# Performance work log

Measured on AMD Instinct MI355X. Metric: run time of the kernel, lower is better.

The kernel has to match this reference:

```python
import jax, jax.numpy as jnp
import numpy as np

N_NODES = 10000
N_EDGES = 640000
NODE_DIM = 128
EDGE_DIM = 32
OUT_DIM = 128


def setup_inputs() -> dict:
    key = jax.random.key(0)
    k_h, k_e, k_ef, k_w1, k_w2 = jax.random.split(key, 5)
    h = jax.random.normal(k_h, (N_NODES, NODE_DIM), dtype=jnp.float32)
    edge_index = jax.random.randint(k_e, (2, N_EDGES), 0, N_NODES, dtype=jnp.int64)
    edge_features = jax.random.normal(k_ef, (N_EDGES, EDGE_DIM), dtype=jnp.float32)
    in_dim = 2 * NODE_DIM + EDGE_DIM
    # Kaiming-ish init scale for realism
    W1 = jax.random.normal(k_w1, (in_dim, OUT_DIM), dtype=jnp.float32) / np.sqrt(in_dim)
    b1 = jnp.zeros((OUT_DIM,), dtype=jnp.float32)
    W2 = jax.random.normal(k_w2, (OUT_DIM, OUT_DIM), dtype=jnp.float32) / np.sqrt(OUT_DIM)
    b2 = jnp.zeros((OUT_DIM,), dtype=jnp.float32)
    return {"h": h, "edge_index": edge_index, "edge_features": edge_features,
            "n": N_NODES, "W1": W1, "b1": b1, "W2": W2, "b2": b2}


def reference(h, edge_index, edge_features, n, W1, b1, W2, b2):
    rows, cols = edge_index[0], edge_index[1]
    # gather source/target node features + edge features -> [E, 2*node_dim+edge_dim]
    msg_input = jnp.concatenate([h[rows], h[cols], edge_features], axis=-1)
    hidden = jax.nn.relu(msg_input @ W1 + b1)   # [E, out_dim]
    messages = hidden @ W2 + b2                 # [E, out_dim]
    # scatter-add messages onto destination rows -> [n, out_dim]
    out = jax.ops.segment_sum(messages, rows, num_segments=n)
    return out
```

## Files before the change

kernel.cpp:

```cpp
#include <hip/hip_runtime.h>
#include <hip/hip_bf16.h>


typedef __attribute__((ext_vector_type(8))) short bf16x8;
typedef __attribute__((ext_vector_type(4))) float f32x4;

#define ND 128
#define ED 32
#define CH 64
#define INV_WSCALE 0.0625f

__device__ __forceinline__ short f2bf(float x) {
  unsigned int u = __float_as_uint(x);
  unsigned int r = (u + 0x7FFFu + ((u >> 16) & 1u)) >> 16;
  return (short)r;
}

__device__ __forceinline__ float bf2f(short s) {
  return __uint_as_float(((unsigned int)(unsigned short)s) << 16);
}

__device__ __forceinline__ f32x4 bf8lo(bf16x8 v) {
  f32x4 r;
  #pragma unroll
  for (int j = 0; j < 4; ++j) r[j] = bf2f(v[j]);
  return r;
}
__device__ __forceinline__ f32x4 bf8hi(bf16x8 v) {
  f32x4 r;
  #pragma unroll
  for (int j = 0; j < 4; ++j) r[j] = bf2f(v[4 + j]);
  return r;
}

__device__ __forceinline__ int pk_fp8x4(float a, float b, float c, float d) {
  int w = __builtin_amdgcn_cvt_pk_fp8_f32(a, b, 0, false);
  w = __builtin_amdgcn_cvt_pk_fp8_f32(c, d, w, true);
  return w;
}

__device__ __forceinline__ int swz(int c) {
  int ct = c >> 4, cc = c & 15;
  return (ct >> 2) * 64 + (cc >> 2) * 16 + (ct & 3) * 4 + (cc & 3);
}

__global__ __launch_bounds__(256) void prep_hist_kernel(
    const float* __restrict__ W1, const float* __restrict__ W2,
    const void* __restrict__ ei, int* __restrict__ counts,
    unsigned int* __restrict__ rc, short* __restrict__ w12t,
    long long* __restrict__ w1eA8, short* __restrict__ w2t, int E) {
  int b = blockIdx.x;
  if (b < 128) {
    int t = b * 256 + threadIdx.x;
    if (t < 256 * 128) {
      int np = t >> 7, k = t & 127;
      float v = (np < 128) ? W1[k * 128 + np] : W1[(128 + k) * 128 + (np - 128)];
      w12t[t] = f2bf(v);
    }
    if (t < 128 * 128) {
      int n = t >> 7, k = t & 127;
      w2t[t] = f2bf(W2[k * 128 + n]);
    }
    if (t < 8 * 64) {
      int ct = t >> 6, lane = t & 63;
      int li = lane & 15, lg = lane >> 4;
      float v[8];
      #pragma unroll
      for (int j = 0; j < 8; ++j)
        v[j] = W1[(256 + lg * 8 + j) * 128 + ct * 16 + li] * 16.f;
      int lo = pk_fp8x4(v[0], v[1], v[2], v[3]);
      int hi = pk_fp8x4(v[4], v[5], v[6], v[7]);
      w1eA8[ct * 64 + lane] = (long long)(unsigned int)lo |
                              ((long long)(unsigned int)hi << 32);
    }
  } else {
    int e = (b - 128) * 256 + threadIdx.x;
    if (e < E) {
      const unsigned int* u = (const unsigned int*)ei;
      int is64 = 1;
      #pragma unroll
      for (int i = 0; i < 16; ++i)
        if (u[2 * i + 1] != 0u) is64 = 0;
      int r, c;
      if (is64) {
        r = (int)((const long long*)ei)[e];
        c = (int)((const long long*)ei)[(long long)E + e];
      } else {
        r = ((const int*)ei)[e];
        c = ((const int*)ei)[E + e];
      }
      atomicAdd(&counts[r], 1);
      rc[e] = ((unsigned int)r << 16) | (unsigned int)c;
    }
  }
}

__global__ __launch_bounds__(1024) void scan_kernel(const int* __restrict__ counts,
                                                    int* __restrict__ row_ptr,
                                                    int* __restrict__ cur, int n) {
  __shared__ int wtot[16];
  int tid = threadIdx.x;
  int lane = tid & 63, w = tid >> 6;
  int base_i = tid * 16;
  int c[16];
  int tot = 0;
  #pragma unroll
  for (int j = 0; j < 16; ++j) {
    int i = base_i + j;
    c[j] = (i < n) ? counts[i] : 0;
    tot += c[j];
  }
  int x = tot;
  #pragma unroll
  for (int d = 1; d < 64; d <<= 1) {
    int t = __shfl_up(x, d);
    if (lane >= d) x += t;
  }
  if (lane == 63) wtot[w] = x;
  __syncthreads();
  if (w == 0) {
    int y = (lane < 16) ? wtot[lane] : 0;
    #pragma unroll
    for (int d = 1; d < 16; d <<= 1) {
      int t = __shfl_up(y, d);
      if (lane >= d) y += t;
    }
    if (lane < 16) wtot[lane] = y;
  }
  __syncthreads();
  int waveoff = (w == 0) ? 0 : wtot[w - 1];
  int run = waveoff + x - tot;
  if (tid == 0) row_ptr[0] = 0;
  #pragma unroll
  for (int j = 0; j < 16; ++j) {
    int i = base_i + j;
    if (i < n) {
      cur[i] = run;
      run += c[j];
      row_ptr[i + 1] = run;
    }
  }
}

__global__ __launch_bounds__(256, 4) void scatter_sg_kernel(
    const float* __restrict__ ef, const int* __restrict__ row_ptr,
    int* __restrict__ cur, const unsigned int* __restrict__ rc,
    const float* __restrict__ h, const short* __restrict__ w12t,
    const float* __restrict__ b1, unsigned char* __restrict__ efb,
    unsigned short* __restrict__ ccol, int2* __restrict__ cb,
    float* __restrict__ s2, short* __restrict__ g2, int N, int E, int nchunks) {
  int b = blockIdx.x;
  int SGB = (N + 63) >> 6;
  int SCB = (2 * E + 255) >> 8;
  if (b < SGB) {
    int lane = threadIdx.x & 63, w = threadIdx.x >> 6;
    int li = lane & 15, lg = lane >> 4;
    int base = b * 64 + w * 16;
    int rowm = base + li;
    if (rowm >= N) rowm = N - 1;
    float breg[8];
    #pragma unroll
    for (int nt = 0; nt < 8; ++nt) breg[nt] = b1[nt * 16 + li];
    f32x4 acc[16];
    #pragma unroll
    for (int nt = 0; nt < 16; ++nt) acc[nt] = (f32x4){0.f, 0.f, 0.f, 0.f};
    #pragma unroll
    for (int kc = 0; kc < 4; ++kc) {
      f32x4 f0 = *(const f32x4*)(h + (size_t)rowm * ND + kc * 32 + lg * 8);
      f32x4 f1 = *(const f32x4*)(h + (size_t)rowm * ND + kc * 32 + lg * 8 + 4);
      bf16x8 a;
      #pragma unroll
      for (int j = 0; j < 4; ++j) { a[j] = f2bf(f0[j]); a[4 + j] = f2bf(f1[j]); }
      #pragma unroll
      for (int nt = 0; nt < 16; ++nt) {
        bf16x8 bb = *(const bf16x8*)(w12t + (nt * 16 + li) * 128 + kc * 32 + lg * 8);
        acc[nt] = __builtin_amdgcn_mfma_f32_16x16x32_bf16(a, bb, acc[nt], 0, 0, 0);
      }
    }
    #pragma unroll
    for (int nt = 0; nt < 16; ++nt)
      #pragma unroll
      for (int r = 0; r < 4; ++r) {
        int row = base + lg * 4 + r;
        if (row < N) {
          if (nt < 8) {
            s2[(size_t)row * 128 + swz(nt * 16 + li)] = acc[nt][r] + breg[nt];
          } else {
            g2[(size_t)row * 128 + swz((nt - 8) * 16 + li)] = f2bf(acc[nt][r]);
          }
        }
      }
  } else if (b < SGB + SCB) {
    int gt = (b - SGB) * 256 + threadIdx.x;
    int e = gt >> 1, part = gt & 1;
    if (e < E) {
      unsigned int p = rc[e];
      int r = (int)(p >> 16), c = (int)(p & 0xffffu);
      int pos0 = 0;
      if (part == 0) pos0 = atomicAdd(&cur[r], 1);
      int lane = threadIdx.x & 63;
      int pos = __shfl(pos0, lane - part);
      const float* ep = ef + (size_t)e * ED + part * 16;
      f32x4 x0 = *(const f32x4*)(ep);
      f32x4 x1 = *(const f32x4*)(ep + 4);
      f32x4 x2 = *(const f32x4*)(ep + 8);
      f32x4 x3 = *(const f32x4*)(ep + 12);
      int4 ob;
      ob.x = pk_fp8x4(x0[0], x0[1], x0[2], x0[3]);
      ob.y = pk_fp8x4(x1[0], x1[1], x1[2], x1[3]);
      ob.z = pk_fp8x4(x2[0], x2[1], x2[2], x2[3]);
      ob.w = pk_fp8x4(x3[0], x3[1], x3[2], x3[3]);
      *(int4*)(efb + (size_t)pos * ED + part * 16) = ob;
      if (part == 0) ccol[pos] = (unsigned short)c;
    }
  } else {
    int k = (b - SGB - SCB) * 256 + threadIdx.x;
    if (k < nchunks) {
      int t0 = k * CH, t1 = t0 + CH;
      int lo = 0, hi = N;
      while (lo < hi) { int mid = (lo + hi) >> 1; if (row_ptr[mid] < t0) lo = mid + 1; else hi = mid; }
      int na = lo;
      hi = N;
      while (lo < hi) { int mid = (lo + hi) >> 1; if (row_ptr[mid] < t1) lo = mid + 1; else hi = mid; }
      cb[k] = make_int2(na, lo);
    }
  }
}

__global__ __launch_bounds__(128, 4) void layer1_kernel(
    const float* __restrict__ s2, const short* __restrict__ g2,
    const unsigned char* __restrict__ efb, const unsigned short* __restrict__ ccol,
    const long long* __restrict__ w1eA8, const int* __restrict__ row_ptr,
    const int2* __restrict__ cb, float* __restrict__ hsum) {
  int2 bounds = cb[blockIdx.x];
  int na = bounds.x, nb = bounds.y;
  if (na >= nb) return;
  int lane = threadIdx.x & 63;
  int w = threadIdx.x >> 6;
  int li = lane & 15, lg = lane >> 4;

  long long wa[4];
  #pragma unroll
  for (int nt = 0; nt < 4; ++nt)
    wa[nt] = w1eA8[(w * 4 + nt) * 64 + lane];

  for (int n = na; n < nb; ++n) {
    int rp = row_ptr[n], rpe = row_ptr[n + 1];
    int deg = rpe - rp;
    f32x4 sreg[4];
    #pragma unroll
    for (int nt = 0; nt < 4; ++nt)
      sreg[nt] = *(const f32x4*)(s2 + (size_t)n * 128 + w * 64 + lg * 16 + nt * 4);
    f32x4 psum[4];
    #pragma unroll
    for (int nt = 0; nt < 4; ++nt) psum[nt] = (f32x4){0.f, 0.f, 0.f, 0.f};

    int ntiles = (deg + 15) >> 4;
    int last = rpe - 1;
    auto ldpos = [&](int t) {
      int p = rp + t * 16 + li;
      return p > last ? last : p;
    };

    int pA = ldpos(0), pB = ldpos(1);
    int cA = ccol[pA], cB = ccol[pB];
    long long eA = *(const long long*)(efb + (size_t)pA * ED + lg * 8);
    long long eB = *(const long long*)(efb + (size_t)pB * ED + lg * 8);
    const short* gpA = g2 + (size_t)cA * 128 + w * 64 + lg * 16;
    bf16x8 gA0 = *(const bf16x8*)gpA;
    bf16x8 gA1 = *(const bf16x8*)(gpA + 8);

    for (int t = 0; t < ntiles; ++t) {
      const short* gpB = g2 + (size_t)cB * 128 + w * 64 + lg * 16;
      bf16x8 gB0 = *(const bf16x8*)gpB;
      bf16x8 gB1 = *(const bf16x8*)(gpB + 8);
      int pC = ldpos(t + 2);
      int cC = ccol[pC];
      long long eC = *(const long long*)(efb + (size_t)pC * ED + lg * 8);
      f32x4 a0 = __builtin_amdgcn_mfma_f32_16x16x32_fp8_fp8(wa[0], eA, (f32x4){0.f,0.f,0.f,0.f}, 0, 0, 0);
      f32x4 a1 = __builtin_amdgcn_mfma_f32_16x16x32_fp8_fp8(wa[1], eA, (f32x4){0.f,0.f,0.f,0.f}, 0, 0, 0);
      f32x4 a2 = __builtin_amdgcn_mfma_f32_16x16x32_fp8_fp8(wa[2], eA, (f32x4){0.f,0.f,0.f,0.f}, 0, 0, 0);
      f32x4 a3 = __builtin_amdgcn_mfma_f32_16x16x32_fp8_fp8(wa[3], eA, (f32x4){0.f,0.f,0.f,0.f}, 0, 0, 0);
      if ((t * 16 + li) < deg) {
        f32x4 g0 = bf8lo(gA0), g1 = bf8hi(gA0), g2v = bf8lo(gA1), g3 = bf8hi(gA1);
        #pragma unroll
        for (int r = 0; r < 4; ++r) {
          float v0 = fmaf(a0[r], INV_WSCALE, sreg[0][r] + g0[r]);
          float v1 = fmaf(a1[r], INV_WSCALE, sreg[1][r] + g1[r]);
          float v2 = fmaf(a2[r], INV_WSCALE, sreg[2][r] + g2v[r]);
          float v3 = fmaf(a3[r], INV_WSCALE, sreg[3][r] + g3[r]);
          psum[0][r] += (v0 > 0.f ? v0 : 0.f);
          psum[1][r] += (v1 > 0.f ? v1 : 0.f);
          psum[2][r] += (v2 > 0.f ? v2 : 0.f);
          psum[3][r] += (v3 > 0.f ? v3 : 0.f);
        }
      }
      cB = cC; eA = eB; eB = eC;
      gA0 = gB0; gA1 = gB1;
    }

    #pragma unroll
    for (int nt = 0; nt < 4; ++nt)
      #pragma unroll
      for (int r = 0; r < 4; ++r) {
        float v = psum[nt][r];
        v += __shfl_xor(v, 1);
        v += __shfl_xor(v, 2);
        v += __shfl_xor(v, 4);
        v += __shfl_xor(v, 8);
        psum[nt][r] = v;
      }
    if (li == 0) {
      #pragma unroll
      for (int nt = 0; nt < 4; ++nt)
        *(f32x4*)(hsum + (size_t)n * 128 + w * 64 + nt * 16 + lg * 4) = psum[nt];
    }
  }
}

__global__ __launch_bounds__(256) void out_kernel(const float* __restrict__ hsum,
                                                  const short* __restrict__ w2t,
                                                  const float* __restrict__ b2,
                                                  const int* __restrict__ row_ptr,
                                                  float* __restrict__ out, int N) {
  int lane = threadIdx.x & 63, w = threadIdx.x >> 6;
  int li = lane & 15, lg = lane >> 4;
  int base = blockIdx.x * 64 + w * 16;
  int rowm = base + li;
  if (rowm >= N) rowm = N - 1;
  float breg[8];
  #pragma unroll
  for (int nt = 0; nt < 8; ++nt) breg[nt] = b2[nt * 16 + li];
  f32x4 acc[8];
  #pragma unroll
  for (int nt = 0; nt < 8; ++nt) acc[nt] = (f32x4){0.f, 0.f, 0.f, 0.f};
  #pragma unroll
  for (int kc = 0; kc < 4; ++kc) {
    f32x4 f0 = *(const f32x4*)(hsum + (size_t)rowm * 128 + kc * 32 + lg * 8);
    f32x4 f1 = *(const f32x4*)(hsum + (size_t)rowm * 128 + kc * 32 + lg * 8 + 4);
    bf16x8 a;
    #pragma unroll
    for (int j = 0; j < 4; ++j) { a[j] = f2bf(f0[j]); a[4 + j] = f2bf(f1[j]); }
    #pragma unroll
    for (int nt = 0; nt < 8; ++nt) {
      bf16x8 bb = *(const bf16x8*)(w2t + (nt * 16 + li) * 128 + kc * 32 + lg * 8);
      acc[nt] = __builtin_amdgcn_mfma_f32_16x16x32_bf16(a, bb, acc[nt], 0, 0, 0);
    }
  }
  #pragma unroll
  for (int r = 0; r < 4; ++r) {
    int row = base + lg * 4 + r;
    if (row < N) {
      float dg = (float)(row_ptr[row + 1] - row_ptr[row]);
      #pragma unroll
      for (int nt = 0; nt < 8; ++nt)
        out[(size_t)row * 128 + nt * 16 + li] = acc[nt][r] + dg * breg[nt];
    }
  }
}

extern "C" void kernel_launch(void* const* d_in, const int* in_sizes, int n_in,
                              void* d_out, int out_size, void* d_ws, size_t ws_size,
                              hipStream_t stream) {
  const float* h  = (const float*)d_in[0];
  const void*  ei = d_in[1];
  const float* ef = (const float*)d_in[2];
  const float* W1 = (const float*)d_in[4];
  const float* b1 = (const float*)d_in[5];
  const float* W2 = (const float*)d_in[6];
  const float* b2 = (const float*)d_in[7];
  float* out = (float*)d_out;
  int N = in_sizes[0] / ND;
  int E = in_sizes[2] / ED;
  int nchunks = (E + CH - 1) / CH;

  char* ws = (char*)d_ws;
  size_t off = 0;
  auto alloc = [&](size_t bytes) {
    size_t o = off;
    off = (off + bytes + 255) & ~(size_t)255;
    return o;
  };
  int*            counts  = (int*)(ws + alloc((size_t)N * 4));
  int*            row_ptr = (int*)(ws + alloc((size_t)(N + 1) * 4));
  int*            cur     = (int*)(ws + alloc((size_t)N * 4));
  unsigned int*   rc      = (unsigned int*)(ws + alloc((size_t)E * 4));
  short*          w12t    = (short*)(ws + alloc(256 * 128 * 2));
  long long*      w1eA8   = (long long*)(ws + alloc(8 * 64 * 8));
  short*          w2t     = (short*)(ws + alloc(128 * 128 * 2));
  float*          s2      = (float*)(ws + alloc((size_t)N * 128 * 4));
  short*          g2      = (short*)(ws + alloc((size_t)N * 128 * 2));
  float*          hsumb   = (float*)(ws + alloc((size_t)N * 128 * 4));
  unsigned char*  efb     = (unsigned char*)(ws + alloc((size_t)E * ED));
  unsigned short* ccol    = (unsigned short*)(ws + alloc((size_t)E * 2));
  int2*           cbb     = (int2*)(ws + alloc((size_t)nchunks * 8));

  int SGB = (N + 63) >> 6;
  int SCB = (2 * E + 255) >> 8;
  int CBB = (nchunks + 255) >> 8;

  hipMemsetAsync(counts, 0, (size_t)N * 4, stream);
  prep_hist_kernel<<<128 + (E + 255) / 256, 256, 0, stream>>>(
      W1, W2, ei, counts, rc, w12t, w1eA8, w2t, E);
  scan_kernel<<<1, 1024, 0, stream>>>(counts, row_ptr, cur, N);
  scatter_sg_kernel<<<SGB + SCB + CBB, 256, 0, stream>>>(
      ef, row_ptr, cur, rc, h, w12t, b1, efb, ccol, cbb, s2, g2, N, E, nchunks);
  layer1_kernel<<<nchunks, 128, 0, stream>>>(s2, g2, efb, ccol, w1eA8, row_ptr, cbb, hsumb);
  out_kernel<<<(N + 63) / 64, 256, 0, stream>>>(hsumb, w2t, b2, row_ptr, out, N);
}
```

Measured before the change: 158.7 us.

## Use histogram ranks for CSR placement, pack edge records, one block per node

The histogram atomic now also returns each edge's rank within its row. The scatter pass computes its CSR position as row_ptr[r]+rank[e], which removes the second atomicAdd pass over a cursor array. Edge features (fp8) and the column index are packed into one 64-byte record so layer1 reads them together. Layer1 now launches one block per node instead of edge-count chunks, which drops the binary-search chunk-bounds step. In exchange it writes an extra rank array and doubles edge-record size, with 28 bytes of zero padding per record, which adds memory traffic.

```diff
diff --git a/kernel.cpp b/kernel.cpp
--- a/kernel.cpp
+++ b/kernel.cpp
@@ -7,7 +7,7 @@
 
 #define ND 128
 #define ED 32
-#define CH 64
+#define RECB 64
 #define INV_WSCALE 0.0625f
 
 __device__ __forceinline__ short f2bf(float x) {
@@ -47,8 +47,9 @@
 __global__ __launch_bounds__(256) void prep_hist_kernel(
     const float* __restrict__ W1, const float* __restrict__ W2,
     const void* __restrict__ ei, int* __restrict__ counts,
-    unsigned int* __restrict__ rc, short* __restrict__ w12t,
-    long long* __restrict__ w1eA8, short* __restrict__ w2t, int E) {
+    int* __restrict__ rank, unsigned int* __restrict__ rc,
+    short* __restrict__ w12t, long long* __restrict__ w1eA8,
+    short* __restrict__ w2t, int E) {
   int b = blockIdx.x;
   if (b < 128) {
     int t = b * 256 + threadIdx.x;
@@ -89,15 +90,14 @@
         r = ((const int*)ei)[e];
         c = ((const int*)ei)[E + e];
       }
-      atomicAdd(&counts[r], 1);
+      rank[e] = atomicAdd(&counts[r], 1);
       rc[e] = ((unsigned int)r << 16) | (unsigned int)c;
     }
   }
 }
 
 __global__ __launch_bounds__(1024) void scan_kernel(const int* __restrict__ counts,
-                                                    int* __restrict__ row_ptr,
-                                                    int* __restrict__ cur, int n) {
+                                                    int* __restrict__ row_ptr, int n) {
   __shared__ int wtot[16];
   int tid = threadIdx.x;
   int lane = tid & 63, w = tid >> 6;
@@ -135,7 +135,6 @@
   for (int j = 0; j < 16; ++j) {
     int i = base_i + j;
     if (i < n) {
-      cur[i] = run;
       run += c[j];
       row_ptr[i + 1] = run;
     }
@@ -144,14 +143,12 @@
 
 __global__ __launch_bounds__(256, 4) void scatter_sg_kernel(
     const float* __restrict__ ef, const int* __restrict__ row_ptr,
-    int* __restrict__ cur, const unsigned int* __restrict__ rc,
+    const int* __restrict__ rank, const unsigned int* __restrict__ rc,
     const float* __restrict__ h, const short* __restrict__ w12t,
     const float* __restrict__ b1, unsigned char* __restrict__ efb,
-    unsigned short* __restrict__ ccol, int2* __restrict__ cb,
-    float* __restrict__ s2, short* __restrict__ g2, int N, int E, int nchunks) {
+    float* __restrict__ s2, short* __restrict__ g2, int N, int E) {
   int b = blockIdx.x;
   int SGB = (N + 63) >> 6;
-  int SCB = (2 * E + 255) >> 8;
   if (b < SGB) {
     int lane = threadIdx.x & 63, w = threadIdx.x >> 6;
     int li = lane & 15, lg = lane >> 4;
@@ -190,16 +187,13 @@
           }
         }
       }
-  } else if (b < SGB + SCB) {
+  } else {
     int gt = (b - SGB) * 256 + threadIdx.x;
     int e = gt >> 1, part = gt & 1;
     if (e < E) {
       unsigned int p = rc[e];
       int r = (int)(p >> 16), c = (int)(p & 0xffffu);
-      int pos0 = 0;
-      if (part == 0) pos0 = atomicAdd(&cur[r], 1);
-      int lane = threadIdx.x & 63;
-      int pos = __shfl(pos0, lane - part);
+      int pos = row_ptr[r] + rank[e];
       const float* ep = ef + (size_t)e * ED + part * 16;
       f32x4 x0 = *(const f32x4*)(ep);
       f32x4 x1 = *(const f32x4*)(ep + 4);
@@ -210,111 +204,109 @@
       ob.y = pk_fp8x4(x1[0], x1[1], x1[2], x1[3]);
       ob.z = pk_fp8x4(x2[0], x2[1], x2[2], x2[3]);
       ob.w = pk_fp8x4(x3[0], x3[1], x3[2], x3[3]);
-      *(int4*)(efb + (size_t)pos * ED + part * 16) = ob;
-      if (part == 0) ccol[pos] = (unsigned short)c;
-    }
-  } else {
-    int k = (b - SGB - SCB) * 256 + threadIdx.x;
-    if (k < nchunks) {
-      int t0 = k * CH, t1 = t0 + CH;
-      int lo = 0, hi = N;
-      while (lo < hi) { int mid = (lo + hi) >> 1; if (row_ptr[mid] < t0) lo = mid + 1; else hi = mid; }
-      int na = lo;
-      hi = N;
-      while (lo < hi) { int mid = (lo + hi) >> 1; if (row_ptr[mid] < t1) lo = mid + 1; else hi = mid; }
-      cb[k] = make_int2(na, lo);
+      unsigned char* rec = efb + (size_t)pos * RECB;
+      *(int4*)(rec + part * 16) = ob;
+      *(int4*)(rec + 32 + part * 16) = make_int4(part == 0 ? c : 0, 0, 0, 0);
     }
   }
 }
 
 __global__ __launch_bounds__(128, 4) void layer1_kernel(
     const float* __restrict__ s2, const short* __restrict__ g2,
-    const unsigned char* __restrict__ efb, const unsigned short* __restrict__ ccol,
-    const long long* __restrict__ w1eA8, const int* __restrict__ row_ptr,
-    const int2* __restrict__ cb, float* __restrict__ hsum) {
-  int2 bounds = cb[blockIdx.x];
-  int na = bounds.x, nb = bounds.y;
-  if (na >= nb) return;
+    const unsigned char* __restrict__ efb, const long long* __restrict__ w1eA8,
+    const int* __restrict__ row_ptr, float* __restrict__ hsum) {
+  int node = blockIdx.x;
   int lane = threadIdx.x & 63;
   int w = threadIdx.x >> 6;
   int li = lane & 15, lg = lane >> 4;
+  int rp = row_ptr[node], rpe = row_ptr[node + 1];
+  int deg = rpe - rp;
+
+  if (deg == 0) {
+    if (li == 0) {
+      #pragma unroll
+      for (int nt = 0; nt < 4; ++nt)
+        *(f32x4*)(hsum + (size_t)node * 128 + w * 64 + nt * 16 + lg * 4) =
+            (f32x4){0.f, 0.f, 0.f, 0.f};
+    }
+    return;
+  }
 
   long long wa[4];
   #pragma unroll
   for (int nt = 0; nt < 4; ++nt)
     wa[nt] = w1eA8[(w * 4 + nt) * 64 + lane];
-
-  for (int n = na; n < nb; ++n) {
-    int rp = row_ptr[n], rpe = row_ptr[n + 1];
-    int deg = rpe - rp;
-    f32x4 sreg[4];
+  f32x4 sreg[4];
+  #pragma unroll
+  for (int nt = 0; nt < 4; ++nt)
+    sreg[nt] = *(const f32x4*)(s2 + (size_t)node * 128 + w * 64 + lg * 16 + nt * 4);
+  f32x4 psum[4];
+  #pragma unroll
+  for (int nt = 0; nt < 4; ++nt) psum[nt] = (f32x4){0.f, 0.f, 0.f, 0.f};
+
+  int ntiles = (deg + 15) >> 4;
+  int last = rpe - 1;
+  auto ldpos = [&](int t) {
+    int p = rp + t * 16 + li;
+    return p > last ? last : p;
+  };
+
+  const unsigned char* recA = efb + (size_t)ldpos(0) * RECB;
+  const unsigned char* recB = efb + (size_t)ldpos(1) * RECB;
+  long long eA = *(const long long*)(recA + lg * 8);
+  int cA = *(const int*)(recA + 32);
+  long long eB = *(const long long*)(recB + lg * 8);
+  int cB = *(const int*)(recB + 32);
+  const short* gpA = g2 + (size_t)cA * 128 + w * 64 + lg * 16;
+  bf16x8 gA0 = *(const bf16x8*)gpA;
+  bf16x8 gA1 = *(const bf16x8*)(gpA + 8);
+
+  for (int t = 0; t < ntiles; ++t) {
+    const short* gpB = g2 + (size_t)cB * 128 + w * 64 + lg * 16;
+    bf16x8 gB0 = *(const bf16x8*)gpB;
+    bf16x8 gB1 = *(const bf16x8*)(gpB + 8);
+    const unsigned char* recC = efb + (size_t)ldpos(t + 2) * RECB;
+    long long eC = *(const long long*)(recC + lg * 8);
+    int cC = *(const int*)(recC + 32);
+    f32x4 a0 = __builtin_amdgcn_mfma_f32_16x16x32_fp8_fp8(wa[0], eA, (f32x4){0.f,0.f,0.f,0.f}, 0, 0, 0);
+    f32x4 a1 = __builtin_amdgcn_mfma_f32_16x16x32_fp8_fp8(wa[1], eA, (f32x4){0.f,0.f,0.f,0.f}, 0, 0, 0);
+    f32x4 a2 = __builtin_amdgcn_mfma_f32_16x16x32_fp8_fp8(wa[2], eA, (f32x4){0.f,0.f,0.f,0.f}, 0, 0, 0);
+    f32x4 a3 = __builtin_amdgcn_mfma_f32_16x16x32_fp8_fp8(wa[3], eA, (f32x4){0.f,0.f,0.f,0.f}, 0, 0, 0);
+    if ((t * 16 + li) < deg) {
+      f32x4 g0 = bf8lo(gA0), g1 = bf8hi(gA0), g2v = bf8lo(gA1), g3 = bf8hi(gA1);
+      #pragma unroll
+      for (int r = 0; r < 4; ++r) {
+        float v0 = fmaf(a0[r], INV_WSCALE, sreg[0][r] + g0[r]);
+        float v1 = fmaf(a1[r], INV_WSCALE, sreg[1][r] + g1[r]);
+        float v2 = fmaf(a2[r], INV_WSCALE, sreg[2][r] + g2v[r]);
+        float v3 = fmaf(a3[r], INV_WSCALE, sreg[3][r] + g3[r]);
+        psum[0][r] += (v0 > 0.f ? v0 : 0.f);
+        psum[1][r] += (v1 > 0.f ? v1 : 0.f);
+        psum[2][r] += (v2 > 0.f ? v2 : 0.f);
+        psum[3][r] += (v3 > 0.f ? v3 : 0.f);
+      }
+    }
+    eA = eB; cB2: ;
+    eB = eC;
+    cA = cB; cB = cC;
+    gA0 = gB0; gA1 = gB1;
+  }
+
+  #pragma unroll
+  for (int nt = 0; nt < 4; ++nt)
+    #pragma unroll
+    for (int r = 0; r < 4; ++r) {
+      float v = psum[nt][r];
+      v += __shfl_xor(v, 1);
+      v += __shfl_xor(v, 2);
+      v += __shfl_xor(v, 4);
+      v += __shfl_xor(v, 8);
+      psum[nt][r] = v;
+    }
+  if (li == 0) {
     #pragma unroll
     for (int nt = 0; nt < 4; ++nt)
-      sreg[nt] = *(const f32x4*)(s2 + (size_t)n * 128 + w * 64 + lg * 16 + nt * 4);
-    f32x4 psum[4];
-    #pragma unroll
-    for (int nt = 0; nt < 4; ++nt) psum[nt] = (f32x4){0.f, 0.f, 0.f, 0.f};
-
-    int ntiles = (deg + 15) >> 4;
-    int last = rpe - 1;
-    auto ldpos = [&](int t) {
-      int p = rp + t * 16 + li;
-      return p > last ? last : p;
-    };
-
-    int pA = ldpos(0), pB = ldpos(1);
-    int cA = ccol[pA], cB = ccol[pB];
-    long long eA = *(const long long*)(efb + (size_t)pA * ED + lg * 8);
-    long long eB = *(const long long*)(efb + (size_t)pB * ED + lg * 8);
-    const short* gpA = g2 + (size_t)cA * 128 + w * 64 + lg * 16;
-    bf16x8 gA0 = *(const bf16x8*)gpA;
-    bf16x8 gA1 = *(const bf16x8*)(gpA + 8);
-
-    for (int t = 0; t < ntiles; ++t) {
-      const short* gpB = g2 + (size_t)cB * 128 + w * 64 + lg * 16;
-      bf16x8 gB0 = *(const bf16x8*)gpB;
-      bf16x8 gB1 = *(const bf16x8*)(gpB + 8);
-      int pC = ldpos(t + 2);
-      int cC = ccol[pC];
-      long long eC = *(const long long*)(efb + (size_t)pC * ED + lg * 8);
-      f32x4 a0 = __builtin_amdgcn_mfma_f32_16x16x32_fp8_fp8(wa[0], eA, (f32x4){0.f,0.f,0.f,0.f}, 0, 0, 0);
-      f32x4 a1 = __builtin_amdgcn_mfma_f32_16x16x32_fp8_fp8(wa[1], eA, (f32x4){0.f,0.f,0.f,0.f}, 0, 0, 0);
-      f32x4 a2 = __builtin_amdgcn_mfma_f32_16x16x32_fp8_fp8(wa[2], eA, (f32x4){0.f,0.f,0.f,0.f}, 0, 0, 0);
-      f32x4 a3 = __builtin_amdgcn_mfma_f32_16x16x32_fp8_fp8(wa[3], eA, (f32x4){0.f,0.f,0.f,0.f}, 0, 0, 0);
-      if ((t * 16 + li) < deg) {
-        f32x4 g0 = bf8lo(gA0), g1 = bf8hi(gA0), g2v = bf8lo(gA1), g3 = bf8hi(gA1);
-        #pragma unroll
-        for (int r = 0; r < 4; ++r) {
-          float v0 = fmaf(a0[r], INV_WSCALE, sreg[0][r] + g0[r]);
-          float v1 = fmaf(a1[r], INV_WSCALE, sreg[1][r] + g1[r]);
-          float v2 = fmaf(a2[r], INV_WSCALE, sreg[2][r] + g2v[r]);
-          float v3 = fmaf(a3[r], INV_WSCALE, sreg[3][r] + g3[r]);
-          psum[0][r] += (v0 > 0.f ? v0 : 0.f);
-          psum[1][r] += (v1 > 0.f ? v1 : 0.f);
-          psum[2][r] += (v2 > 0.f ? v2 : 0.f);
-          psum[3][r] += (v3 > 0.f ? v3 : 0.f);
-        }
-      }
-      cB = cC; eA = eB; eB = eC;
-      gA0 = gB0; gA1 = gB1;
-    }
-
-    #pragma unroll
-    for (int nt = 0; nt < 4; ++nt)
-      #pragma unroll
-      for (int r = 0; r < 4; ++r) {
-        float v = psum[nt][r];
-        v += __shfl_xor(v, 1);
-        v += __shfl_xor(v, 2);
-        v += __shfl_xor(v, 4);
-        v += __shfl_xor(v, 8);
-        psum[nt][r] = v;
-      }
-    if (li == 0) {
-      #pragma unroll
-      for (int nt = 0; nt < 4; ++nt)
-        *(f32x4*)(hsum + (size_t)n * 128 + w * 64 + nt * 16 + lg * 4) = psum[nt];
-    }
+      *(f32x4*)(hsum + (size_t)node * 128 + w * 64 + nt * 16 + lg * 4) = psum[nt];
   }
 }
 
@@ -372,7 +364,6 @@
   float* out = (float*)d_out;
   int N = in_sizes[0] / ND;
   int E = in_sizes[2] / ED;
-  int nchunks = (E + CH - 1) / CH;
 
   char* ws = (char*)d_ws;
   size_t off = 0;
@@ -381,30 +372,27 @@
     off = (off + bytes + 255) & ~(size_t)255;
     return o;
   };
-  int*            counts  = (int*)(ws + alloc((size_t)N * 4));
-  int*            row_ptr = (int*)(ws + alloc((size_t)(N + 1) * 4));
-  int*            cur     = (int*)(ws + alloc((size_t)N * 4));
-  unsigned int*   rc      = (unsigned int*)(ws + alloc((size_t)E * 4));
-  short*          w12t    = (short*)(ws + alloc(256 * 128 * 2));
-  long long*      w1eA8   = (long long*)(ws + alloc(8 * 64 * 8));
-  short*          w2t     = (short*)(ws + alloc(128 * 128 * 2));
-  float*          s2      = (float*)(ws + alloc((size_t)N * 128 * 4));
-  short*          g2      = (short*)(ws + alloc((size_t)N * 128 * 2));
-  float*          hsumb   = (float*)(ws + alloc((size_t)N * 128 * 4));
-  unsigned char*  efb     = (unsigned char*)(ws + alloc((size_t)E * ED));
-  unsigned short* ccol    = (unsigned short*)(ws + alloc((size_t)E * 2));
-  int2*           cbb     = (int2*)(ws + alloc((size_t)nchunks * 8));
+  int*           counts  = (int*)(ws + alloc((size_t)N * 4));
+  int*           row_ptr = (int*)(ws + alloc((size_t)(N + 1) * 4));
+  int*           rank    = (int*)(ws + alloc((size_t)E * 4));
+  unsigned int*  rc      = (unsigned int*)(ws + alloc((size_t)E * 4));
+  short*         w12t    = (short*)(ws + alloc(256 * 128 * 2));
+  long long*     w1eA8   = (long long*)(ws + alloc(8 * 64 * 8));
+  short*         w2t     = (short*)(ws + alloc(128 * 128 * 2));
+  float*         s2      = (float*)(ws + alloc((size_t)N * 128 * 4));
+  short*         g2      = (short*)(ws + alloc((size_t)N * 128 * 2));
+  float*         hsumb   = (float*)(ws + alloc((size_t)N * 128 * 4));
+  unsigned char* efb     = (unsigned char*)(ws + alloc((size_t)E * RECB));
 
   int SGB = (N + 63) >> 6;
   int SCB = (2 * E + 255) >> 8;
-  int CBB = (nchunks + 255) >> 8;
 
   hipMemsetAsync(counts, 0, (size_t)N * 4, stream);
   prep_hist_kernel<<<128 + (E + 255) / 256, 256, 0, stream>>>(
-      W1, W2, ei, counts, rc, w12t, w1eA8, w2t, E);
-  scan_kernel<<<1, 1024, 0, stream>>>(counts, row_ptr, cur, N);
-  scatter_sg_kernel<<<SGB + SCB + CBB, 256, 0, stream>>>(
-      ef, row_ptr, cur, rc, h, w12t, b1, efb, ccol, cbb, s2, g2, N, E, nchunks);
-  layer1_kernel<<<nchunks, 128, 0, stream>>>(s2, g2, efb, ccol, w1eA8, row_ptr, cbb, hsumb);
+      W1, W2, ei, counts, rank, rc, w12t, w1eA8, w2t, E);
+  scan_kernel<<<1, 1024, 0, stream>>>(counts, row_ptr, N);
+  scatter_sg_kernel<<<SGB + SCB, 256, 0, stream>>>(
+      ef, row_ptr, rank, rc, h, w12t, b1, efb, s2, g2, N, E);
+  layer1_kernel<<<N, 128, 0, stream>>>(s2, g2, efb, w1eA8, row_ptr, hsumb);
   out_kernel<<<(N + 63) / 64, 256, 0, stream>>>(hsumb, w2t, b2, row_ptr, out, N);
 }
```

Result: faster. 139.9 us (-11.8%).
